# Kernel tuning notes

Measured on AMD Instinct MI355X. Metric: run time of the kernel, lower is better.

## Reference

```python
import jax, jax.numpy as jnp
import numpy as np

N, E, D, H = 50000, 800000, 64, 4


def setup_inputs() -> dict:
    key = jax.random.key(0)
    ks = jax.random.split(key, 12)
    w = lambda k, shape: jax.random.normal(k, shape, jnp.float32) * 0.05
    return {
        "nfeats": jax.random.normal(ks[0], (N, D), jnp.float32),
        "efeats": jax.random.normal(ks[1], (E, D), jnp.float32),
        "src": jax.random.randint(ks[2], (E,), 0, N),
        "dst": jax.random.randint(ks[3], (E,), 0, N),
        "W_ni": w(ks[4], (D, H * D)),
        "W_nj": w(ks[5], (D, H * D)),
        "W_fij": w(ks[6], (D, H * D)),
        "bias_e": jnp.zeros((H * D,), jnp.float32),
        "attn": w(ks[7], (H, D)),
        "W_src": w(ks[8], (D, H * D)),
        "W_mlp_node": w(ks[9], (H * D, D)),
        "b_mlp_node": jnp.zeros((D,), jnp.float32),
        "W_mlp_edge": w(ks[10], (H * D, D)),
        "b_mlp_edge": jnp.zeros((D,), jnp.float32),
    }


def reference(nfeats, efeats, src, dst, W_ni, W_nj, W_fij, bias_e, attn,
              W_src, W_mlp_node, b_mlp_node, W_mlp_edge, b_mlp_edge):
    n, d = nfeats.shape
    h = attn.shape[0]
    # DGL EGATConv: edge logits from src node, dst node and edge features
    f_ni = (nfeats @ W_ni)[src]            # [E, H*D] gather src
    f_nj = (nfeats @ W_nj)[dst]            # [E, H*D] gather dst
    f_fij = efeats @ W_fij                 # [E, H*D]
    f_out = jax.nn.leaky_relu(f_ni + f_nj + f_fij + bias_e, 0.01)
    f_out = f_out.reshape(-1, h, d)        # [E, H, D] new edge feats
    e = jnp.einsum('ehd,hd->eh', f_out, attn)  # [E, H] attention logits
    # edge softmax over incoming edges of each dst node
    e_max = jax.ops.segment_max(e, dst, num_segments=n)
    e_exp = jnp.exp(e - e_max[dst])
    denom = jax.ops.segment_sum(e_exp, dst, num_segments=n)
    a = e_exp / denom[dst]                 # [E, H]
    # weighted message passing: scatter-sum to dst
    h_src = (nfeats @ W_src).reshape(n, h, d)[src]  # [E, H, D]
    h_out = jax.ops.segment_sum(h_src * a[:, :, None], dst, num_segments=n)  # [N, H, D]
    # EGATLayer head-mixing MLPs + ELU
    node = jax.nn.elu(h_out.reshape(n, h * d) @ W_mlp_node + b_mlp_node)
    edge = jax.nn.elu(f_out.reshape(-1, h * d) @ W_mlp_edge + b_mlp_edge)
    return node, edge
```

## Files before the change

kernel.cpp:

```cpp
#include <hip/hip_runtime.h>
#include <hip/hip_bf16.h>

#define N_NODES 50000
#define N_EDGES 800000
#define DD 64
#define HH 4
#define HD 256
#define EB 32
#define CAP 64

typedef __attribute__((ext_vector_type(8))) short bf16x8;
typedef __attribute__((ext_vector_type(4))) float f32x4;

__device__ __forceinline__ short f2bf(float x) {
  return __builtin_bit_cast(short, __float2bfloat16(x));
}
__device__ __forceinline__ float bf2f(unsigned short u) {
  return __builtin_bit_cast(float, (unsigned)u << 16);
}

__global__ __launch_bounds__(256) void k_proj(const float* __restrict__ nfeats,
    const float* __restrict__ W_src, unsigned short* __restrict__ hsrc) {
  __shared__ __align__(16) float Wl[DD * HD];
  const float4* W4 = (const float4*)W_src;
  float4* Wl4 = (float4*)Wl;
#pragma unroll
  for (int i = 0; i < 16; ++i) Wl4[threadIdx.x + i * 256] = W4[threadIdx.x + i * 256];
  __syncthreads();
  const int wave = threadIdx.x >> 6, lane = threadIdx.x & 63;
  for (int n = blockIdx.x * 4 + wave; n < N_NODES; n += gridDim.x * 4) {
    const float4* x4 = (const float4*)(nfeats + n * DD);
    float4 acc = make_float4(0.f, 0.f, 0.f, 0.f);
#pragma unroll
    for (int k4 = 0; k4 < 16; ++k4) {
      float4 xv = x4[k4];
      const float* wr = &Wl[(k4 * 4) * HD + 4 * lane];
      float4 w0 = *(const float4*)(wr);
      float4 w1 = *(const float4*)(wr + HD);
      float4 w2 = *(const float4*)(wr + 2 * HD);
      float4 w3 = *(const float4*)(wr + 3 * HD);
      acc.x += xv.x * w0.x + xv.y * w1.x + xv.z * w2.x + xv.w * w3.x;
      acc.y += xv.x * w0.y + xv.y * w1.y + xv.z * w2.y + xv.w * w3.y;
      acc.z += xv.x * w0.z + xv.y * w1.z + xv.z * w2.z + xv.w * w3.z;
      acc.w += xv.x * w0.w + xv.y * w1.w + xv.z * w2.w + xv.w * w3.w;
    }
    short4 s;
    s.x = f2bf(acc.x); s.y = f2bf(acc.y); s.z = f2bf(acc.z); s.w = f2bf(acc.w);
    *(short4*)&hsrc[n * HD + 4 * lane] = s;
  }
}

__global__ __launch_bounds__(256, 2) void k_edge(
    const float* __restrict__ efeats, const int* __restrict__ src, const int* __restrict__ dst,
    const float* __restrict__ nfeats,
    const float* __restrict__ W_fij, const float* __restrict__ W_ni, const float* __restrict__ W_nj,
    const float* __restrict__ bias_e, const float* __restrict__ attn,
    const float* __restrict__ W_mlp_edge, const float* __restrict__ b_mlp_edge,
    float* __restrict__ eexp, float* __restrict__ edge_out) {
  __shared__ __align__(16) short a_lds[12 * 64 * 8];
  __shared__ __align__(16) short fout_lds[EB * HD];

  const int t = threadIdx.x;
  const int lane = t & 63;
  const int w = t >> 6;
  const int l15 = lane & 15, l4 = lane >> 4;

  bf16x8 wcat[6][4];
#pragma unroll
  for (int ks = 0; ks < 6; ++ks) {
    const float* Wp = ks < 2 ? (W_fij + (ks * 32) * HD)
                             : (ks < 4 ? (W_ni + ((ks - 2) * 32) * HD)
                                       : (W_nj + ((ks - 4) * 32) * HD));
#pragma unroll
    for (int n = 0; n < 4; ++n) {
      bf16x8 a;
#pragma unroll
      for (int i = 0; i < 8; ++i)
        a[i] = f2bf(Wp[(l4 * 8 + i) * HD + (w * 64 + n * 16 + l15)]);
      wcat[ks][n] = a;
    }
  }
  bf16x8 wm[8];
#pragma unroll
  for (int ks = 0; ks < 8; ++ks) {
    bf16x8 b;
#pragma unroll
    for (int i = 0; i < 8; ++i)
      b[i] = f2bf(W_mlp_edge[(ks * 32 + l4 * 8 + i) * 64 + (w * 16 + l15)]);
    wm[ks] = b;
  }
  float bias_r[4], attn_r[4];
#pragma unroll
  for (int n = 0; n < 4; ++n) {
    const int col = w * 64 + n * 16 + l15;
    bias_r[n] = bias_e[col];
    attn_r[n] = attn[col];
  }
  const float bme_r = b_mlp_edge[w * 16 + l15];

  const int fr = t >> 3;
  const int c = t & 7;
  const int fc = c * 8;
  const int msub = fr >> 4, rr = fr & 15, kq = c >> 2, kk = c & 3;
  const int posx = ((rr ^ c) & 15) | (kk << 4);

  for (int tile = blockIdx.x; tile < N_EDGES / EB; tile += gridDim.x) {
    const int base = tile * EB;
    {
      const int srow = src[base + fr], drow = dst[base + fr];
      float4 x0, x1; bf16x8 p;

      x0 = *(const float4*)&efeats[(base + fr) * DD + fc];
      x1 = *(const float4*)&efeats[(base + fr) * DD + fc + 4];
      p[0] = f2bf(x0.x); p[1] = f2bf(x0.y); p[2] = f2bf(x0.z); p[3] = f2bf(x0.w);
      p[4] = f2bf(x1.x); p[5] = f2bf(x1.y); p[6] = f2bf(x1.z); p[7] = f2bf(x1.w);
      ((bf16x8*)a_lds)[(msub * 6 + kq) * 64 + posx] = p;

      x0 = *(const float4*)&nfeats[srow * DD + fc];
      x1 = *(const float4*)&nfeats[srow * DD + fc + 4];
      p[0] = f2bf(x0.x); p[1] = f2bf(x0.y); p[2] = f2bf(x0.z); p[3] = f2bf(x0.w);
      p[4] = f2bf(x1.x); p[5] = f2bf(x1.y); p[6] = f2bf(x1.z); p[7] = f2bf(x1.w);
      ((bf16x8*)a_lds)[(msub * 6 + 2 + kq) * 64 + posx] = p;

      x0 = *(const float4*)&nfeats[drow * DD + fc];
      x1 = *(const float4*)&nfeats[drow * DD + fc + 4];
      p[0] = f2bf(x0.x); p[1] = f2bf(x0.y); p[2] = f2bf(x0.z); p[3] = f2bf(x0.w);
      p[4] = f2bf(x1.x); p[5] = f2bf(x1.y); p[6] = f2bf(x1.z); p[7] = f2bf(x1.w);
      ((bf16x8*)a_lds)[(msub * 6 + 4 + kq) * 64 + posx] = p;
    }
    __syncthreads();

    f32x4 acc[2][4] = {};
#pragma unroll
    for (int m = 0; m < 2; ++m) {
      bf16x8 af[6];
#pragma unroll
      for (int ks = 0; ks < 6; ++ks) {
        const int px = (((lane & 15) ^ (((ks & 1) << 2) | (lane >> 4))) & 15) | ((lane >> 4) << 4);
        af[ks] = ((const bf16x8*)a_lds)[(m * 6 + ks) * 64 + px];
      }
#pragma unroll
      for (int n = 0; n < 4; ++n)
#pragma unroll
        for (int ks = 0; ks < 6; ++ks)
          acc[m][n] = __builtin_amdgcn_mfma_f32_16x16x32_bf16(af[ks], wcat[ks][n], acc[m][n], 0, 0, 0);
    }

#pragma unroll
    for (int m = 0; m < 2; ++m) {
#pragma unroll
      for (int reg = 0; reg < 4; ++reg) {
        const int re = m * 16 + l4 * 4 + reg;
        float p = 0.f;
#pragma unroll
        for (int n = 0; n < 4; ++n) {
          const int col = w * 64 + n * 16 + l15;
          float v = acc[m][n][reg] + bias_r[n];
          v = v >= 0.f ? v : 0.01f * v;
          p += v * attn_r[n];
          int byte = re * 512 + col * 2;
          byte ^= (re & 7) << 4;
          *(short*)((char*)fout_lds + byte) = f2bf(v);
        }
        p += __shfl_xor(p, 1, 64); p += __shfl_xor(p, 2, 64);
        p += __shfl_xor(p, 4, 64); p += __shfl_xor(p, 8, 64);
        if (l15 == 0) {
          eexp[(base + re) * 4 + w] = expf(p);
        }
      }
    }
    __syncthreads();

#pragma unroll
    for (int m = 0; m < 2; ++m) {
      f32x4 acc2 = {};
#pragma unroll
      for (int ks = 0; ks < 8; ++ks) {
        int byte = (m * 16 + l15) * 512 + ks * 64 + l4 * 16;
        byte ^= (l15 & 7) << 4;
        bf16x8 pf = *(const bf16x8*)((char*)fout_lds + byte);
        acc2 = __builtin_amdgcn_mfma_f32_16x16x32_bf16(pf, wm[ks], acc2, 0, 0, 0);
      }
#pragma unroll
      for (int reg = 0; reg < 4; ++reg) {
        float v = acc2[reg] + bme_r;
        v = v > 0.f ? v : (expf(v) - 1.f);
        edge_out[(size_t)(base + m * 16 + l4 * 4 + reg) * DD + w * 16 + l15] = v;
      }
    }
  }
}

__global__ __launch_bounds__(256) void k_fill(const int* __restrict__ dst,
    int* __restrict__ cnt, int* __restrict__ bucket) {
  const int e = blockIdx.x * 256 + threadIdx.x;
  if (e < N_EDGES) {
    const int d = dst[e];
    const int slot = atomicAdd(&cnt[d], 1);
    if (slot < CAP) bucket[d * CAP + slot] = e;
  }
}

__global__ __launch_bounds__(256) void k_aggc(const int* __restrict__ src,
    const int* __restrict__ cnt, const int* __restrict__ bucket,
    const float* __restrict__ eexp, const unsigned short* __restrict__ hsrc_all,
    float* __restrict__ h_out) {
  const int lane = threadIdx.x & 63;
  const int n = (blockIdx.x * 256 + threadIdx.x) >> 6;
  if (n >= N_NODES) return;
  int deg = cnt[n];
  if (deg > CAP) deg = CAP;
  float ex0 = 0.f, ex1 = 0.f, ex2 = 0.f, ex3 = 0.f;
  int s = 0;
  if (lane < deg) {
    const int e = bucket[n * CAP + lane];
    s = src[e];
    const float4 ex = *(const float4*)&eexp[e * 4];
    ex0 = ex.x; ex1 = ex.y; ex2 = ex.z; ex3 = ex.w;
  }
  float d0 = ex0, d1 = ex1, d2 = ex2, d3 = ex3;
#pragma unroll
  for (int off = 32; off; off >>= 1) {
    d0 += __shfl_xor(d0, off, 64); d1 += __shfl_xor(d1, off, 64);
    d2 += __shfl_xor(d2, off, 64); d3 += __shfl_xor(d3, off, 64);
  }
  float a0 = 0.f, a1 = 0.f, a2 = 0.f, a3 = 0.f;
  for (int i = 0; i < deg; ++i) {
    const int si = __shfl(s, i, 64);
    const float w0 = __shfl(ex0, i, 64), w1 = __shfl(ex1, i, 64);
    const float w2 = __shfl(ex2, i, 64), w3 = __shfl(ex3, i, 64);
    const unsigned short* hp = hsrc_all + (size_t)si * HD;
    a0 += w0 * bf2f(hp[lane]);
    a1 += w1 * bf2f(hp[64 + lane]);
    a2 += w2 * bf2f(hp[128 + lane]);
    a3 += w3 * bf2f(hp[192 + lane]);
  }
  float* op = h_out + (size_t)n * HD;
  op[lane]       = d0 > 0.f ? a0 / d0 : 0.f;
  op[64 + lane]  = d1 > 0.f ? a1 / d1 : 0.f;
  op[128 + lane] = d2 > 0.f ? a2 / d2 : 0.f;
  op[192 + lane] = d3 > 0.f ? a3 / d3 : 0.f;
}

__global__ __launch_bounds__(256) void k_node(const float* __restrict__ h_out,
    const float* __restrict__ W, const float* __restrict__ b, float* __restrict__ node) {
  __shared__ __align__(16) float Wl[HD * 64];
  const float4* W4 = (const float4*)W;
  float4* Wl4 = (float4*)Wl;
#pragma unroll
  for (int i = 0; i < 16; ++i) Wl4[threadIdx.x + i * 256] = W4[threadIdx.x + i * 256];
  __syncthreads();
  const int wave = threadIdx.x >> 6, lane = threadIdx.x & 63;
  const float br = b[lane];
  for (int n = blockIdx.x * 4 + wave; n < N_NODES; n += gridDim.x * 4) {
    const float4* h4 = (const float4*)(h_out + n * HD);
    float acc = 0.f;
#pragma unroll 8
    for (int k4 = 0; k4 < 64; ++k4) {
      float4 hv = h4[k4];
      acc += hv.x * Wl[(k4 * 4) * 64 + lane] + hv.y * Wl[(k4 * 4 + 1) * 64 + lane] +
             hv.z * Wl[(k4 * 4 + 2) * 64 + lane] + hv.w * Wl[(k4 * 4 + 3) * 64 + lane];
    }
    float v = acc + br;
    node[n * DD + lane] = v > 0.f ? v : (expf(v) - 1.f);
  }
}

extern "C" void kernel_launch(void* const* d_in, const int* in_sizes, int n_in,
                              void* d_out, int out_size, void* d_ws, size_t ws_size,
                              hipStream_t stream) {
  const float* nfeats     = (const float*)d_in[0];
  const float* efeats     = (const float*)d_in[1];
  const int*   src        = (const int*)d_in[2];
  const int*   dst        = (const int*)d_in[3];
  const float* W_ni       = (const float*)d_in[4];
  const float* W_nj       = (const float*)d_in[5];
  const float* W_fij      = (const float*)d_in[6];
  const float* bias_e     = (const float*)d_in[7];
  const float* attn       = (const float*)d_in[8];
  const float* W_src      = (const float*)d_in[9];
  const float* W_mlp_node = (const float*)d_in[10];
  const float* b_mlp_node = (const float*)d_in[11];
  const float* W_mlp_edge = (const float*)d_in[12];
  const float* b_mlp_edge = (const float*)d_in[13];

  float* node_out = (float*)d_out;
  float* edge_out = node_out + (size_t)N_NODES * DD;

  char* wsb = (char*)d_ws;
  unsigned short* hsrc_bf = (unsigned short*)wsb;
  float* eexp  = (float*)(wsb + 25600000);
  float* h_out = (float*)(wsb + 38400000);
  int*   cnt    = (int*)(wsb + 89600000);
  int*   bucket = (int*)(wsb + 89800000);

  k_proj<<<512, 256, 0, stream>>>(nfeats, W_src, hsrc_bf);
  k_edge<<<1024, 256, 0, stream>>>(efeats, src, dst, nfeats,
                                   W_fij, W_ni, W_nj, bias_e, attn,
                                   W_mlp_edge, b_mlp_edge, eexp, edge_out);
  hipMemsetAsync(cnt, 0, (size_t)N_NODES * sizeof(int), stream);
  k_fill<<<(N_EDGES + 255) / 256, 256, 0, stream>>>(dst, cnt, bucket);
  k_aggc<<<(N_NODES * 64 + 255) / 256, 256, 0, stream>>>(src, cnt, bucket, eexp, hsrc_bf, h_out);
  k_node<<<512, 256, 0, stream>>>(h_out, W_mlp_node, b_mlp_node, node_out);
}
```

Baseline: 600.2 us.

## Fuse fill into projection, fuse aggregation with node MLP, enlarge edge tile

After: 1.348 ms. +124.5%, slower.

```diff
diff --git a/kernel.cpp b/kernel.cpp
--- a/kernel.cpp
+++ b/kernel.cpp
@@ -6,7 +6,7 @@
 #define DD 64
 #define HH 4
 #define HD 256
-#define EB 32
+#define EB 64
 #define CAP 64
 
 typedef __attribute__((ext_vector_type(8))) short bf16x8;
@@ -19,8 +19,21 @@
   return __builtin_bit_cast(float, (unsigned)u << 16);
 }
 
-__global__ __launch_bounds__(256) void k_proj(const float* __restrict__ nfeats,
-    const float* __restrict__ W_src, unsigned short* __restrict__ hsrc) {
+#define PROJ_BLKS 512
+#define FILL_BLKS ((N_EDGES + 255) / 256)
+
+__global__ __launch_bounds__(256) void k_pre(const float* __restrict__ nfeats,
+    const float* __restrict__ W_src, unsigned short* __restrict__ hsrc,
+    const int* __restrict__ dst, int* __restrict__ cnt, int* __restrict__ bucket) {
+  if (blockIdx.x >= PROJ_BLKS) {
+    const int e = (blockIdx.x - PROJ_BLKS) * 256 + threadIdx.x;
+    if (e < N_EDGES) {
+      const int d = dst[e];
+      const int slot = atomicAdd(&cnt[d], 1);
+      if (slot < CAP) bucket[d * CAP + slot] = e;
+    }
+    return;
+  }
   __shared__ __align__(16) float Wl[DD * HD];
   const float4* W4 = (const float4*)W_src;
   float4* Wl4 = (float4*)Wl;
@@ -28,7 +41,7 @@
   for (int i = 0; i < 16; ++i) Wl4[threadIdx.x + i * 256] = W4[threadIdx.x + i * 256];
   __syncthreads();
   const int wave = threadIdx.x >> 6, lane = threadIdx.x & 63;
-  for (int n = blockIdx.x * 4 + wave; n < N_NODES; n += gridDim.x * 4) {
+  for (int n = blockIdx.x * 4 + wave; n < N_NODES; n += PROJ_BLKS * 4) {
     const float4* x4 = (const float4*)(nfeats + n * DD);
     float4 acc = make_float4(0.f, 0.f, 0.f, 0.f);
 #pragma unroll
@@ -57,7 +70,7 @@
     const float* __restrict__ bias_e, const float* __restrict__ attn,
     const float* __restrict__ W_mlp_edge, const float* __restrict__ b_mlp_edge,
     float* __restrict__ eexp, float* __restrict__ edge_out) {
-  __shared__ __align__(16) short a_lds[12 * 64 * 8];
+  __shared__ __align__(16) short a_lds[24 * 64 * 8];
   __shared__ __align__(16) short fout_lds[EB * HD];
 
   const int t = threadIdx.x;
@@ -98,45 +111,46 @@
   }
   const float bme_r = b_mlp_edge[w * 16 + l15];
 
-  const int fr = t >> 3;
-  const int c = t & 7;
-  const int fc = c * 8;
-  const int msub = fr >> 4, rr = fr & 15, kq = c >> 2, kk = c & 3;
-  const int posx = ((rr ^ c) & 15) | (kk << 4);
+  const int fr = t >> 2;
+  const int c2 = t & 3;
+  const int fc = c2 * 16;
+  const int msub = fr >> 4, rr = fr & 15;
+  const int kq = c2 >> 1, kk0 = (c2 & 1) * 2;
+  const int posx0 = ((rr ^ (kq * 4 + kk0)) & 15) | (kk0 << 4);
+  const int posx1 = ((rr ^ (kq * 4 + kk0 + 1)) & 15) | ((kk0 + 1) << 4);
 
   for (int tile = blockIdx.x; tile < N_EDGES / EB; tile += gridDim.x) {
     const int base = tile * EB;
     {
       const int srow = src[base + fr], drow = dst[base + fr];
-      float4 x0, x1; bf16x8 p;
-
-      x0 = *(const float4*)&efeats[(base + fr) * DD + fc];
-      x1 = *(const float4*)&efeats[(base + fr) * DD + fc + 4];
-      p[0] = f2bf(x0.x); p[1] = f2bf(x0.y); p[2] = f2bf(x0.z); p[3] = f2bf(x0.w);
-      p[4] = f2bf(x1.x); p[5] = f2bf(x1.y); p[6] = f2bf(x1.z); p[7] = f2bf(x1.w);
-      ((bf16x8*)a_lds)[(msub * 6 + kq) * 64 + posx] = p;
-
-      x0 = *(const float4*)&nfeats[srow * DD + fc];
-      x1 = *(const float4*)&nfeats[srow * DD + fc + 4];
-      p[0] = f2bf(x0.x); p[1] = f2bf(x0.y); p[2] = f2bf(x0.z); p[3] = f2bf(x0.w);
-      p[4] = f2bf(x1.x); p[5] = f2bf(x1.y); p[6] = f2bf(x1.z); p[7] = f2bf(x1.w);
-      ((bf16x8*)a_lds)[(msub * 6 + 2 + kq) * 64 + posx] = p;
-
-      x0 = *(const float4*)&nfeats[drow * DD + fc];
-      x1 = *(const float4*)&nfeats[drow * DD + fc + 4];
-      p[0] = f2bf(x0.x); p[1] = f2bf(x0.y); p[2] = f2bf(x0.z); p[3] = f2bf(x0.w);
-      p[4] = f2bf(x1.x); p[5] = f2bf(x1.y); p[6] = f2bf(x1.z); p[7] = f2bf(x1.w);
-      ((bf16x8*)a_lds)[(msub * 6 + 4 + kq) * 64 + posx] = p;
-    }
-    __syncthreads();
-
-    f32x4 acc[2][4] = {};
-#pragma unroll
-    for (int m = 0; m < 2; ++m) {
+      const float* rows[3] = { efeats + (size_t)(base + fr) * DD + fc,
+                               nfeats + (size_t)srow * DD + fc,
+                               nfeats + (size_t)drow * DD + fc };
+#pragma unroll
+      for (int mat = 0; mat < 3; ++mat) {
+        float4 x0 = *(const float4*)(rows[mat]);
+        float4 x1 = *(const float4*)(rows[mat] + 4);
+        float4 x2 = *(const float4*)(rows[mat] + 8);
+        float4 x3 = *(const float4*)(rows[mat] + 12);
+        bf16x8 p0, p1;
+        p0[0] = f2bf(x0.x); p0[1] = f2bf(x0.y); p0[2] = f2bf(x0.z); p0[3] = f2bf(x0.w);
+        p0[4] = f2bf(x1.x); p0[5] = f2bf(x1.y); p0[6] = f2bf(x1.z); p0[7] = f2bf(x1.w);
+        p1[0] = f2bf(x2.x); p1[1] = f2bf(x2.y); p1[2] = f2bf(x2.z); p1[3] = f2bf(x2.w);
+        p1[4] = f2bf(x3.x); p1[5] = f2bf(x3.y); p1[6] = f2bf(x3.z); p1[7] = f2bf(x3.w);
+        const int ch = (msub * 6 + mat * 2 + kq) * 64;
+        ((bf16x8*)a_lds)[ch + posx0] = p0;
+        ((bf16x8*)a_lds)[ch + posx1] = p1;
+      }
+    }
+    __syncthreads();
+
+    f32x4 acc[4][4] = {};
+#pragma unroll
+    for (int m = 0; m < 4; ++m) {
       bf16x8 af[6];
 #pragma unroll
       for (int ks = 0; ks < 6; ++ks) {
-        const int px = (((lane & 15) ^ (((ks & 1) << 2) | (lane >> 4))) & 15) | ((lane >> 4) << 4);
+        const int px = ((l15 ^ (((ks & 1) << 2) | l4)) & 15) | (l4 << 4);
         af[ks] = ((const bf16x8*)a_lds)[(m * 6 + ks) * 64 + px];
       }
 #pragma unroll
@@ -147,7 +161,7 @@
     }
 
 #pragma unroll
-    for (int m = 0; m < 2; ++m) {
+    for (int m = 0; m < 4; ++m) {
 #pragma unroll
       for (int reg = 0; reg < 4; ++reg) {
         const int re = m * 16 + l4 * 4 + reg;
@@ -172,7 +186,7 @@
     __syncthreads();
 
 #pragma unroll
-    for (int m = 0; m < 2; ++m) {
+    for (int m = 0; m < 4; ++m) {
       f32x4 acc2 = {};
 #pragma unroll
       for (int ks = 0; ks < 8; ++ks) {
@@ -191,78 +205,58 @@
   }
 }
 
-__global__ __launch_bounds__(256) void k_fill(const int* __restrict__ dst,
-    int* __restrict__ cnt, int* __restrict__ bucket) {
-  const int e = blockIdx.x * 256 + threadIdx.x;
-  if (e < N_EDGES) {
-    const int d = dst[e];
-    const int slot = atomicAdd(&cnt[d], 1);
-    if (slot < CAP) bucket[d * CAP + slot] = e;
-  }
-}
-
-__global__ __launch_bounds__(256) void k_aggc(const int* __restrict__ src,
+__global__ __launch_bounds__(256) void k_aggf(const int* __restrict__ src,
     const int* __restrict__ cnt, const int* __restrict__ bucket,
     const float* __restrict__ eexp, const unsigned short* __restrict__ hsrc_all,
-    float* __restrict__ h_out) {
+    const float* __restrict__ W_mlp_node, const float* __restrict__ b_mlp_node,
+    float* __restrict__ node_out) {
+  __shared__ float part[4][64];
   const int lane = threadIdx.x & 63;
-  const int n = (blockIdx.x * 256 + threadIdx.x) >> 6;
-  if (n >= N_NODES) return;
-  int deg = cnt[n];
-  if (deg > CAP) deg = CAP;
-  float ex0 = 0.f, ex1 = 0.f, ex2 = 0.f, ex3 = 0.f;
-  int s = 0;
-  if (lane < deg) {
-    const int e = bucket[n * CAP + lane];
-    s = src[e];
-    const float4 ex = *(const float4*)&eexp[e * 4];
-    ex0 = ex.x; ex1 = ex.y; ex2 = ex.z; ex3 = ex.w;
-  }
-  float d0 = ex0, d1 = ex1, d2 = ex2, d3 = ex3;
-#pragma unroll
-  for (int off = 32; off; off >>= 1) {
-    d0 += __shfl_xor(d0, off, 64); d1 += __shfl_xor(d1, off, 64);
-    d2 += __shfl_xor(d2, off, 64); d3 += __shfl_xor(d3, off, 64);
-  }
-  float a0 = 0.f, a1 = 0.f, a2 = 0.f, a3 = 0.f;
-  for (int i = 0; i < deg; ++i) {
-    const int si = __shfl(s, i, 64);
-    const float w0 = __shfl(ex0, i, 64), w1 = __shfl(ex1, i, 64);
-    const float w2 = __shfl(ex2, i, 64), w3 = __shfl(ex3, i, 64);
-    const unsigned short* hp = hsrc_all + (size_t)si * HD;
-    a0 += w0 * bf2f(hp[lane]);
-    a1 += w1 * bf2f(hp[64 + lane]);
-    a2 += w2 * bf2f(hp[128 + lane]);
-    a3 += w3 * bf2f(hp[192 + lane]);
-  }
-  float* op = h_out + (size_t)n * HD;
-  op[lane]       = d0 > 0.f ? a0 / d0 : 0.f;
-  op[64 + lane]  = d1 > 0.f ? a1 / d1 : 0.f;
-  op[128 + lane] = d2 > 0.f ? a2 / d2 : 0.f;
-  op[192 + lane] = d3 > 0.f ? a3 / d3 : 0.f;
-}
-
-__global__ __launch_bounds__(256) void k_node(const float* __restrict__ h_out,
-    const float* __restrict__ W, const float* __restrict__ b, float* __restrict__ node) {
-  __shared__ __align__(16) float Wl[HD * 64];
-  const float4* W4 = (const float4*)W;
-  float4* Wl4 = (float4*)Wl;
-#pragma unroll
-  for (int i = 0; i < 16; ++i) Wl4[threadIdx.x + i * 256] = W4[threadIdx.x + i * 256];
-  __syncthreads();
-  const int wave = threadIdx.x >> 6, lane = threadIdx.x & 63;
-  const float br = b[lane];
-  for (int n = blockIdx.x * 4 + wave; n < N_NODES; n += gridDim.x * 4) {
-    const float4* h4 = (const float4*)(h_out + n * HD);
-    float acc = 0.f;
-#pragma unroll 8
-    for (int k4 = 0; k4 < 64; ++k4) {
-      float4 hv = h4[k4];
-      acc += hv.x * Wl[(k4 * 4) * 64 + lane] + hv.y * Wl[(k4 * 4 + 1) * 64 + lane] +
-             hv.z * Wl[(k4 * 4 + 2) * 64 + lane] + hv.w * Wl[(k4 * 4 + 3) * 64 + lane];
-    }
-    float v = acc + br;
-    node[n * DD + lane] = v > 0.f ? v : (expf(v) - 1.f);
+  const int q = threadIdx.x >> 6;
+  bf16x8 wn8[8];
+#pragma unroll
+  for (int i = 0; i < 8; ++i) {
+    bf16x8 v;
+#pragma unroll
+    for (int j = 0; j < 8; ++j) v[j] = f2bf(W_mlp_node[(q * 64 + i * 8 + j) * 64 + lane]);
+    wn8[i] = v;
+  }
+  const float br = b_mlp_node[lane];
+
+  for (int n = blockIdx.x; n < N_NODES; n += gridDim.x) {
+    int deg = cnt[n];
+    if (deg > CAP) deg = CAP;
+    float ex = 0.f;
+    int s = 0;
+    if (lane < deg) {
+      const int e = bucket[n * CAP + lane];
+      s = src[e];
+      ex = eexp[e * 4 + q];
+    }
+    float d = ex;
+#pragma unroll
+    for (int off = 32; off; off >>= 1) d += __shfl_xor(d, off, 64);
+    float a = 0.f;
+    for (int i = 0; i < deg; ++i) {
+      const int si = __shfl(s, i, 64);
+      const float wgt = __shfl(ex, i, 64);
+      a += wgt * bf2f(hsrc_all[(size_t)si * HD + q * 64 + lane]);
+    }
+    const float hval = d > 0.f ? a / d : 0.f;
+    float out = 0.f;
+#pragma unroll
+    for (int i = 0; i < 8; ++i)
+#pragma unroll
+      for (int j = 0; j < 8; ++j)
+        out += __shfl(hval, i * 8 + j, 64) * bf2f((unsigned short)wn8[i][j]);
+    part[q][lane] = out;
+    __syncthreads();
+    if (q == 0) {
+      float v = part[0][lane] + part[1][lane] + part[2][lane] + part[3][lane] + br;
+      v = v > 0.f ? v : (expf(v) - 1.f);
+      node_out[(size_t)n * DD + lane] = v;
+    }
+    __syncthreads();
   }
 }
 
@@ -289,17 +283,15 @@
 
   char* wsb = (char*)d_ws;
   unsigned short* hsrc_bf = (unsigned short*)wsb;
-  float* eexp  = (float*)(wsb + 25600000);
-  float* h_out = (float*)(wsb + 38400000);
+  float* eexp   = (float*)(wsb + 25600000);
   int*   cnt    = (int*)(wsb + 89600000);
   int*   bucket = (int*)(wsb + 89800000);
 
-  k_proj<<<512, 256, 0, stream>>>(nfeats, W_src, hsrc_bf);
+  hipMemsetAsync(cnt, 0, (size_t)N_NODES * sizeof(int), stream);
+  k_pre<<<PROJ_BLKS + FILL_BLKS, 256, 0, stream>>>(nfeats, W_src, hsrc_bf, dst, cnt, bucket);
   k_edge<<<1024, 256, 0, stream>>>(efeats, src, dst, nfeats,
                                    W_fij, W_ni, W_nj, bias_e, attn,
                                    W_mlp_edge, b_mlp_edge, eexp, edge_out);
-  hipMemsetAsync(cnt, 0, (size_t)N_NODES * sizeof(int), stream);
-  k_fill<<<(N_EDGES + 255) / 256, 256, 0, stream>>>(dst, cnt, bucket);
-  k_aggc<<<(N_NODES * 64 + 255) / 256, 256, 0, stream>>>(src, cnt, bucket, eexp, hsrc_bf, h_out);
-  k_node<<<512, 256, 0, stream>>>(h_out, W_mlp_node, b_mlp_node, node_out);
-}
+  k_aggf<<<2048, 256, 0, stream>>>(src, cnt, bucket, eexp, hsrc_bf,
+                                   W_mlp_node, b_mlp_node, node_out);
+}
```
